# Performance work log

Measured on AMD Instinct MI355X. Metric: run time of the kernel, lower is better.

## Reference

```python
import jax, jax.numpy as jnp
import numpy as np

D_MODEL = 768
NUM_HEADS = 12
D_K = D_MODEL // NUM_HEADS
B, T = 2, 4096


def setup_inputs() -> dict:
    key = jax.random.key(0)
    ks = jax.random.split(key, 5)
    x = jax.random.normal(ks[0], (B, T, D_MODEL), dtype=jnp.float32)
    # causal mask: True = masked (matches masked_fill semantics)
    mask = jnp.triu(jnp.ones((T, T), dtype=bool), k=1)
    W_qkv = jax.random.normal(ks[1], (D_MODEL, 3 * D_MODEL), dtype=jnp.float32) / np.sqrt(D_MODEL)
    b_qkv = jax.random.normal(ks[2], (3 * D_MODEL,), dtype=jnp.float32) * 0.02
    W_out = jax.random.normal(ks[3], (D_MODEL, D_MODEL), dtype=jnp.float32) / np.sqrt(D_MODEL)
    b_out = jax.random.normal(ks[4], (D_MODEL,), dtype=jnp.float32) * 0.02
    return {"x": x, "mask": mask, "W_qkv": W_qkv, "b_qkv": b_qkv, "W_out": W_out, "b_out": b_out}


def reference(x, mask, W_qkv, b_qkv, W_out, b_out):
    Bb, Tt, C = x.shape
    qkv = x @ W_qkv + b_qkv                       # [B,T,3C]
    # torch: reshape(B,T,H,3*d_k).transpose(1,2) then chunk on last dim
    qkv = qkv.reshape(Bb, Tt, NUM_HEADS, 3, D_K)  # split each head's 3*d_k chunk
    qkv = jnp.transpose(qkv, (0, 2, 1, 3, 4))     # [B,H,T,3,d_k]
    q, k, v = qkv[..., 0, :], qkv[..., 1, :], qkv[..., 2, :]
    scores = jnp.einsum('bhqd,bhkd->bhqk', q, k) / np.sqrt(D_K)
    scores = jnp.where(mask[None, None], -jnp.inf, scores)
    attn = jax.nn.softmax(scores, axis=-1)
    context = jnp.einsum('bhqk,bhkd->bhqd', attn, v)
    context = jnp.transpose(context, (0, 2, 1, 3)).reshape(Bb, Tt, C)
    return context @ W_out + b_out
```

## Files before the change

kernel.cpp:

```cpp
#include <hip/hip_runtime.h>
#include <hip/hip_bf16.h>
#include <stdint.h>


typedef __attribute__((ext_vector_type(8))) short bf16x8;
typedef __attribute__((ext_vector_type(4))) short bf16x4;
typedef __attribute__((ext_vector_type(4))) float f32x4;

#define TT 4096
#define NH 12
#define DK 64
#define DMODEL 768
#define NQKV 2304

__device__ __forceinline__ unsigned short f2bf(float f) {
    union { float f; unsigned u; } v; v.f = f;
    unsigned u = v.u;
    return (unsigned short)((u + 0x7fffu + ((u >> 16) & 1u)) >> 16);
}
__device__ __forceinline__ unsigned fbits(float f) {
    union { float f; unsigned u; } v; v.f = f; return v.u;
}
__device__ __forceinline__ unsigned pack_bf2(float a, float b) {
    return __builtin_amdgcn_perm(fbits(b) + 0x8000u, fbits(a) + 0x8000u, 0x07060302u);
}
__device__ __forceinline__ unsigned cvt_pk_bf16(float a, float b) {
    unsigned r;
    asm("v_cvt_pk_bf16_f32 %0, %1, %2" : "=v"(r) : "v"(a), "v"(b));
    return r;
}
__device__ __forceinline__ void glds16(const void* g, void* l) {
    __builtin_amdgcn_global_load_lds(
        (const __attribute__((address_space(1))) void*)g,
        (__attribute__((address_space(3))) void*)l, 16, 0, 0);
}

__global__ __launch_bounds__(256)
void prep(const float* __restrict__ x, unsigned short* __restrict__ xb,
          const float* __restrict__ Wq, unsigned short* __restrict__ Wqt,
          const float* __restrict__ Wo, unsigned short* __restrict__ Wot) {
    int b = blockIdx.x;
    if (b < 6144) {
        int i = (b * 256 + threadIdx.x) * 4;
        float4 v = *(const float4*)(x + i);
        uint2 u;
        u.x = pack_bf2(v.x, v.y);
        u.y = pack_bf2(v.z, v.w);
        *(uint2*)(xb + i) = u;
        return;
    }
    __shared__ unsigned short tile[64][65];
    const float* W; unsigned short* Wt; int K, N, bx, by;
    if (b < 6144 + 432) {
        int bb = b - 6144; bx = bb % 36; by = bb / 36;
        W = Wq; Wt = Wqt; K = DMODEL; N = NQKV;
    } else {
        int bb = b - 6576; bx = bb % 12; by = bb / 12;
        W = Wo; Wt = Wot; K = DMODEL; N = DMODEL;
    }
    int k0 = by * 64, n0 = bx * 64;
    int c = threadIdx.x & 63;
    int r0 = threadIdx.x >> 6;
    for (int p = 0; p < 16; ++p) {
        int r = r0 + p * 4;
        tile[r][c] = f2bf(W[(size_t)(k0 + r) * N + n0 + c]);
    }
    __syncthreads();
    for (int p = 0; p < 16; ++p) {
        int n = r0 + p * 4;
        Wt[(size_t)(n0 + n) * K + k0 + c] = tile[c][n];
    }
}

__global__ __launch_bounds__(256, 3)
void gemm_qkv(const unsigned short* __restrict__ Amat, const unsigned short* __restrict__ Bmat,
              const float* __restrict__ bias, unsigned short* __restrict__ qb,
              unsigned short* __restrict__ kb, unsigned short* __restrict__ vtb) {
    __shared__ unsigned short As[192 * 64];
    __shared__ unsigned short Bs[128 * 64];
    const int K = DMODEL;
    int bid = (int)blockIdx.y * 64 + (int)blockIdx.x;
    int idx = bid >> 3;
    int n0 = ((bid & 7) * 8 + (idx & 7)) * 128;
    int m0 = (idx >> 3) * 192;
    int tid = threadIdx.x, lane = tid & 63, w = tid >> 6;
    int wm = (w >> 1) * 96, wn = (w & 1) * 64;
    int quad = lane >> 4, lc = lane & 15;

    int gc8 = ((lane & 7) ^ (lane >> 3)) * 8;
    int arow0 = w * 48 + (lane >> 3);
    int brow0 = w * 32 + (lane >> 3);
    const unsigned short* agp0 = Amat + (size_t)(m0 + arow0) * K + gc8;
    const unsigned short* bgp0 = Bmat + (size_t)(n0 + brow0) * K + gc8;
    unsigned short* alp0 = &As[w * 6 * 512];
    unsigned short* blp0 = &Bs[w * 4 * 512];

    int foff[2];
    for (int h = 0; h < 2; ++h)
        foff[h] = lc * 64 + (((quad + 4 * h) ^ (lc & 7)) * 8);

    f32x4 acc[6][4];
    for (int a = 0; a < 6; ++a)
        for (int b2 = 0; b2 < 4; ++b2) acc[a][b2] = (f32x4){0.f, 0.f, 0.f, 0.f};

    for (int k0 = 0; k0 < K; k0 += 64) {
        {
            const unsigned short* ag = agp0;
            for (int p = 0; p < 6; ++p) {
                glds16(ag, alp0 + p * 512);
                ag += 8 * DMODEL;
            }
            const unsigned short* bg = bgp0;
            for (int p = 0; p < 4; ++p) {
                glds16(bg, blp0 + p * 512);
                bg += 8 * DMODEL;
            }
            agp0 += 64; bgp0 += 64;
        }
        __syncthreads();
        bf16x8 bfr[4][2];
        for (int nt = 0; nt < 4; ++nt)
            for (int h = 0; h < 2; ++h)
                bfr[nt][h] = *(const bf16x8*)(&Bs[wn * 64 + nt * 1024 + foff[h]]);
        for (int mt = 0; mt < 6; ++mt) {
            bf16x8 af0 = *(const bf16x8*)(&As[wm * 64 + mt * 1024 + foff[0]]);
            bf16x8 af1 = *(const bf16x8*)(&As[wm * 64 + mt * 1024 + foff[1]]);
            for (int nt = 0; nt < 4; ++nt) {
                acc[mt][nt] = __builtin_amdgcn_mfma_f32_16x16x32_bf16(
                    af0, bfr[nt][0], acc[mt][nt], 0, 0, 0);
                acc[mt][nt] = __builtin_amdgcn_mfma_f32_16x16x32_bf16(
                    af1, bfr[nt][1], acc[mt][nt], 0, 0, 0);
            }
        }
        __syncthreads();
    }
    const float c2q = 0.18033688f;
    for (int mt = 0; mt < 6; ++mt) {
        int colv = m0 + wm + mt * 16 + quad * 4;
        float4 bv = *(const float4*)(bias + colv);
        int h = colv / 192;
        int r = colv - h * 192;
        int which = r >> 6;
        int d0 = r & 63;
        for (int nt = 0; nt < 4; ++nt) {
            int tok = n0 + wn + nt * 16 + lc;
            int b = tok >> 12, t = tok & 4095;
            size_t bh = (size_t)(b * NH + h);
            float v0 = acc[mt][nt][0] + bv.x, v1 = acc[mt][nt][1] + bv.y;
            float v2 = acc[mt][nt][2] + bv.z, v3 = acc[mt][nt][3] + bv.w;
            if (which == 0) {
                uint2 u;
                u.x = cvt_pk_bf16(v0 * c2q, v1 * c2q);
                u.y = cvt_pk_bf16(v2 * c2q, v3 * c2q);
                *(uint2*)(qb + (bh * TT + t) * DK + d0) = u;
            } else if (which == 1) {
                uint2 u;
                u.x = cvt_pk_bf16(v0, v1);
                u.y = cvt_pk_bf16(v2, v3);
                *(uint2*)(kb + (bh * TT + t) * DK + d0) = u;
            } else {
                unsigned short* vp = vtb + (bh * DK + d0) * TT + t;
                vp[0] = f2bf(v0); vp[TT] = f2bf(v1);
                vp[2 * TT] = f2bf(v2); vp[3 * TT] = f2bf(v3);
            }
        }
    }
}

template <bool DIAG>
__device__ __forceinline__ void flash_tile(const unsigned short* __restrict__ Kb,
                                           const unsigned short* __restrict__ Vb,
                                           bf16x8 qf0, bf16x8 qf1,
                                           f32x4 (&o)[4], f32x4& ol,
                                           int kt, int q_lo, int quad, int lc) {
    int c0 = quad ^ (lc & 7);
    int sw = lc & 7;
    const bf16x4 ones = {(short)0x3F80, (short)0x3F80, (short)0x3F80, (short)0x3F80};
    for (int ktile = 0; ktile < 4; ++ktile) {
        bf16x8 kf0 = *(const bf16x8*)(&Kb[(ktile * 16 + lc) * 64 + c0 * 8]);
        bf16x8 kf1 = *(const bf16x8*)(&Kb[(ktile * 16 + lc) * 64 + (c0 ^ 4) * 8]);
        f32x4 s = (f32x4){0.f, 0.f, 0.f, 0.f};
        __builtin_amdgcn_s_setprio(1);
        s = __builtin_amdgcn_mfma_f32_16x16x32_bf16(kf0, qf0, s, 0, 0, 0);
        s = __builtin_amdgcn_mfma_f32_16x16x32_bf16(kf1, qf1, s, 0, 0, 0);
        __builtin_amdgcn_s_setprio(0);
        float p[4];
        if (DIAG) {
            int key0 = kt + ktile * 16 + quad * 4;
            int qcol = q_lo + lc;
            for (int i = 0; i < 4; ++i) {
                float e = __builtin_amdgcn_exp2f(s[i]);
                if (key0 + i > qcol) e = 0.f;
                p[i] = e;
            }
        } else {
            for (int i = 0; i < 4; ++i) p[i] = __builtin_amdgcn_exp2f(s[i]);
        }
        union { uint2 u; bf16x4 v; } pc;
        pc.u.x = cvt_pk_bf16(p[0], p[1]);
        pc.u.y = cvt_pk_bf16(p[2], p[3]);
        int c8 = (ktile * 2 + (quad >> 1)) ^ sw;
        int voff = c8 * 8 + (quad & 1) * 4;
        __builtin_amdgcn_s_setprio(1);
        ol = __builtin_amdgcn_mfma_f32_16x16x16bf16_1k(ones, pc.v, ol, 0, 0, 0);
        for (int dt = 0; dt < 4; ++dt) {
            bf16x4 vf = *(const bf16x4*)(&Vb[(dt * 16 + lc) * 64 + voff]);
            o[dt] = __builtin_amdgcn_mfma_f32_16x16x16bf16_1k(vf, pc.v, o[dt], 0, 0, 0);
        }
        __builtin_amdgcn_s_setprio(0);
    }
}

__global__ __launch_bounds__(256)
void flash_attn(const unsigned short* __restrict__ qbuf,
                const unsigned short* __restrict__ kbuf,
                const unsigned short* __restrict__ vtbuf,
                unsigned short* __restrict__ ctx) {
    __shared__ unsigned short Ks[2][64 * 64];
    __shared__ unsigned short Vs[2][64 * 64];
    int bh = blockIdx.x;
    int qblk = 63 - (int)blockIdx.y;
    int tid = threadIdx.x, lane = tid & 63, w = tid >> 6;
    int quad = lane >> 4, lc = lane & 15;
    const size_t base = (size_t)bh * TT * DK;
    int col8 = ((lane & 7) ^ (lane >> 3)) * 8;
    size_t hb = (size_t)(bh / NH) * TT * DMODEL + (size_t)(bh % NH) * DK;

    int q_lo = qblk * 64 + w * 16;
    int ntile = qblk + 1;

    int rb = (w & 1) * 4;
    const unsigned short* sgp[4];
    int stepEls;
    if (w < 2) {
        const unsigned short* kb0 = kbuf + base + (size_t)(lane >> 3) * DK + col8;
        for (int r = 0; r < 4; ++r) sgp[r] = kb0 + (size_t)((rb + r) * 8) * DK;
        stepEls = 64 * DK;
    } else {
        const unsigned short* vb0 = vtbuf + base + (size_t)(lane >> 3) * TT + col8;
        for (int r = 0; r < 4; ++r) sgp[r] = vb0 + (size_t)((rb + r) * 8) * TT;
        stepEls = 64;
    }

    bf16x8 qf0, qf1;
    {
        const unsigned short* qp = qbuf + base + (size_t)(q_lo + lc) * DK;
        qf0 = *(const bf16x8*)(qp + quad * 8);
        qf1 = *(const bf16x8*)(qp + 32 + quad * 8);
    }
    f32x4 o[4];
    for (int dt = 0; dt < 4; ++dt) o[dt] = (f32x4){0.f, 0.f, 0.f, 0.f};
    f32x4 ol = (f32x4){0.f, 0.f, 0.f, 0.f};

    {
        if (w < 2)
            for (int r = 0; r < 4; ++r) {
                glds16(sgp[r], &Ks[0][(rb + r) * 512]);
                sgp[r] += stepEls;
            }
        else
            for (int r = 0; r < 4; ++r) {
                glds16(sgp[r], &Vs[0][(rb + r) * 512]);
                sgp[r] += stepEls;
            }
    }
    __syncthreads();

    for (int ti = 0; ti < ntile; ++ti) {
        int cur = ti & 1;
        if (ti + 1 < ntile) {
            if (w < 2)
                for (int r = 0; r < 4; ++r) {
                    glds16(sgp[r], &Ks[cur ^ 1][(rb + r) * 512]);
                    sgp[r] += stepEls;
                }
            else
                for (int r = 0; r < 4; ++r) {
                    glds16(sgp[r], &Vs[cur ^ 1][(rb + r) * 512]);
                    sgp[r] += stepEls;
                }
        }
        int kt = ti * 64;
        if (ti == ntile - 1)
            flash_tile<true>(&Ks[cur][0], &Vs[cur][0], qf0, qf1, o, ol,
                             kt, q_lo, quad, lc);
        else
            flash_tile<false>(&Ks[cur][0], &Vs[cur][0], qf0, qf1, o, ol,
                              kt, q_lo, quad, lc);
        __syncthreads();
    }

    float inv = 1.f / ol[0];
    int t = q_lo + lc;
    unsigned short* cp = ctx + hb + (size_t)t * DMODEL;
    for (int dt = 0; dt < 4; ++dt) {
        uint2 u;
        u.x = cvt_pk_bf16(o[dt][0] * inv, o[dt][1] * inv);
        u.y = cvt_pk_bf16(o[dt][2] * inv, o[dt][3] * inv);
        *(uint2*)(cp + dt * 16 + quad * 4) = u;
    }
}

__global__ __launch_bounds__(256, 4)
void gemm_out(const unsigned short* __restrict__ Amat, const unsigned short* __restrict__ Bmat,
              const float* __restrict__ bias, float* __restrict__ out) {
    __shared__ unsigned short S[(64 + 128) * 64];
    const int K = DMODEL;
    int bid = (int)blockIdx.y * 64 + (int)blockIdx.x;
    int idx = bid >> 3;
    int n0 = ((bid & 7) * 8 + (idx & 7)) * 128;
    int m0 = (idx >> 3) * 64;
    int tid = threadIdx.x, lane = tid & 63, w = tid >> 6;
    int wm = (w & 1) * 32, wn = (w >> 1) * 64;
    int quad = lane >> 4, lc = lane & 15;

    const unsigned short* gp[6]; unsigned short* lp[6];
    for (int p = 0; p < 6; ++p) {
        int c = (w * 6 + p) * 64 + lane;
        if (c < 512) {
            int row = c >> 3, gc = (c & 7) ^ (row & 7);
            gp[p] = Amat + (size_t)(m0 + row) * K + gc * 8;
        } else {
            int cb = c - 512;
            int row = cb >> 3, gc = (cb & 7) ^ (row & 7);
            gp[p] = Bmat + (size_t)(n0 + row) * K + gc * 8;
        }
        lp[p] = &S[(w * 6 + p) * 512];
    }
    int foffA[2][2], foffB[4][2];
    for (int mt = 0; mt < 2; ++mt)
        for (int h = 0; h < 2; ++h)
            foffA[mt][h] = (wm + mt * 16 + lc) * 64 + (((quad + 4 * h) ^ (lc & 7)) * 8);
    for (int nt = 0; nt < 4; ++nt)
        for (int h = 0; h < 2; ++h)
            foffB[nt][h] = 4096 + (wn + nt * 16 + lc) * 64 + (((quad + 4 * h) ^ (lc & 7)) * 8);

    f32x4 acc[2][4];
    for (int a = 0; a < 2; ++a)
        for (int b2 = 0; b2 < 4; ++b2) acc[a][b2] = (f32x4){0.f, 0.f, 0.f, 0.f};

    for (int k0 = 0; k0 < K; k0 += 64) {
        for (int p = 0; p < 6; ++p) {
            glds16(gp[p], lp[p]);
            gp[p] += 64;
        }
        __syncthreads();
        bf16x8 af[2][2], bfr[4][2];
        for (int mt = 0; mt < 2; ++mt)
            for (int h = 0; h < 2; ++h) af[mt][h] = *(const bf16x8*)(&S[foffA[mt][h]]);
        for (int nt = 0; nt < 4; ++nt)
            for (int h = 0; h < 2; ++h) bfr[nt][h] = *(const bf16x8*)(&S[foffB[nt][h]]);
        for (int mt = 0; mt < 2; ++mt)
            for (int nt = 0; nt < 4; ++nt) {
                acc[mt][nt] = __builtin_amdgcn_mfma_f32_16x16x32_bf16(
                    af[mt][0], bfr[nt][0], acc[mt][nt], 0, 0, 0);
                acc[mt][nt] = __builtin_amdgcn_mfma_f32_16x16x32_bf16(
                    af[mt][1], bfr[nt][1], acc[mt][nt], 0, 0, 0);
            }
        __syncthreads();
    }
    for (int mt = 0; mt < 2; ++mt) {
        int colv = m0 + wm + mt * 16 + quad * 4;
        float4 bv = *(const float4*)(bias + colv);
        for (int nt = 0; nt < 4; ++nt) {
            int tok = n0 + wn + nt * 16 + lc;
            float4 ov;
            ov.x = acc[mt][nt][0] + bv.x;
            ov.y = acc[mt][nt][1] + bv.y;
            ov.z = acc[mt][nt][2] + bv.z;
            ov.w = acc[mt][nt][3] + bv.w;
            *(float4*)(out + (size_t)tok * DMODEL + colv) = ov;
        }
    }
}

extern "C" void kernel_launch(void* const* d_in, const int* in_sizes, int n_in,
                              void* d_out, int out_size, void* d_ws, size_t ws_size,
                              hipStream_t stream) {
    const float* x     = (const float*)d_in[0];
    const float* W_qkv = (const float*)d_in[2];
    const float* b_qkv = (const float*)d_in[3];
    const float* W_out = (const float*)d_in[4];
    const float* b_out = (const float*)d_in[5];
    float* out = (float*)d_out;

    unsigned short* ws = (unsigned short*)d_ws;
    unsigned short* Wqkv_t = ws;
    unsigned short* Wout_t = Wqkv_t + (size_t)NQKV * DMODEL;
    unsigned short* q_buf  = Wout_t + (size_t)DMODEL * DMODEL;
    unsigned short* k_buf  = q_buf  + (size_t)2 * NH * TT * DK;
    unsigned short* vt_buf = k_buf  + (size_t)2 * NH * TT * DK;
    unsigned short* ctx    = vt_buf + (size_t)2 * NH * TT * DK;
    unsigned short* x_bf   = ctx;

    prep<<<dim3(6720), 256, 0, stream>>>(x, x_bf, W_qkv, Wqkv_t, W_out, Wout_t);
    gemm_qkv<<<dim3((2 * TT) / 128, NQKV / 192), 256, 0, stream>>>(
        Wqkv_t, x_bf, b_qkv, q_buf, k_buf, vt_buf);
    flash_attn<<<dim3(2 * NH, TT / 64), 256, 0, stream>>>(q_buf, k_buf, vt_buf, ctx);
    gemm_out<<<dim3((2 * TT) / 128, DMODEL / 64), 256, 0, stream>>>(
        Wout_t, ctx, b_out, out);
}
```

Before: 255.3 us.

## Double-buffer LDS tiles in QKV and output projection GEMMs

Both projection GEMMs now keep two LDS buffers. The next K-slice is prefetched into the spare buffer while MFMAs run on the current one, and the barrier that sat between load and compute inside the loop is removed. The aim is to hide global-to-LDS load latency behind matrix math. In exchange LDS use doubles, so the launch-bounds occupancy targets drop from 3 to 2 and from 4 to 3 blocks per CU.

```diff
diff --git a/kernel.cpp b/kernel.cpp
--- a/kernel.cpp
+++ b/kernel.cpp
@@ -72,13 +72,14 @@
     }
 }
 
-__global__ __launch_bounds__(256, 3)
+__global__ __launch_bounds__(256, 2)
 void gemm_qkv(const unsigned short* __restrict__ Amat, const unsigned short* __restrict__ Bmat,
               const float* __restrict__ bias, unsigned short* __restrict__ qb,
               unsigned short* __restrict__ kb, unsigned short* __restrict__ vtb) {
-    __shared__ unsigned short As[192 * 64];
-    __shared__ unsigned short Bs[128 * 64];
+    __shared__ unsigned short As[2][192 * 64];
+    __shared__ unsigned short Bs[2][128 * 64];
     const int K = DMODEL;
+    const int NSTEP = K / 64;
     int bid = (int)blockIdx.y * 64 + (int)blockIdx.x;
     int idx = bid >> 3;
     int n0 = ((bid & 7) * 8 + (idx & 7)) * 128;
@@ -92,8 +93,8 @@
     int brow0 = w * 32 + (lane >> 3);
     const unsigned short* agp0 = Amat + (size_t)(m0 + arow0) * K + gc8;
     const unsigned short* bgp0 = Bmat + (size_t)(n0 + brow0) * K + gc8;
-    unsigned short* alp0 = &As[w * 6 * 512];
-    unsigned short* blp0 = &Bs[w * 4 * 512];
+    int alo = w * 6 * 512;
+    int blo = w * 4 * 512;
 
     int foff[2];
     for (int h = 0; h < 2; ++h)
@@ -103,28 +104,31 @@
     for (int a = 0; a < 6; ++a)
         for (int b2 = 0; b2 < 4; ++b2) acc[a][b2] = (f32x4){0.f, 0.f, 0.f, 0.f};
 
-    for (int k0 = 0; k0 < K; k0 += 64) {
-        {
+    {
+        const unsigned short* ag = agp0;
+        for (int p = 0; p < 6; ++p) { glds16(ag, &As[0][alo + p * 512]); ag += 8 * DMODEL; }
+        const unsigned short* bg = bgp0;
+        for (int p = 0; p < 4; ++p) { glds16(bg, &Bs[0][blo + p * 512]); bg += 8 * DMODEL; }
+        agp0 += 64; bgp0 += 64;
+    }
+    __syncthreads();
+
+    for (int step = 0; step < NSTEP; ++step) {
+        int cur = step & 1;
+        if (step + 1 < NSTEP) {
             const unsigned short* ag = agp0;
-            for (int p = 0; p < 6; ++p) {
-                glds16(ag, alp0 + p * 512);
-                ag += 8 * DMODEL;
-            }
+            for (int p = 0; p < 6; ++p) { glds16(ag, &As[cur ^ 1][alo + p * 512]); ag += 8 * DMODEL; }
             const unsigned short* bg = bgp0;
-            for (int p = 0; p < 4; ++p) {
-                glds16(bg, blp0 + p * 512);
-                bg += 8 * DMODEL;
-            }
+            for (int p = 0; p < 4; ++p) { glds16(bg, &Bs[cur ^ 1][blo + p * 512]); bg += 8 * DMODEL; }
             agp0 += 64; bgp0 += 64;
         }
-        __syncthreads();
         bf16x8 bfr[4][2];
         for (int nt = 0; nt < 4; ++nt)
             for (int h = 0; h < 2; ++h)
-                bfr[nt][h] = *(const bf16x8*)(&Bs[wn * 64 + nt * 1024 + foff[h]]);
+                bfr[nt][h] = *(const bf16x8*)(&Bs[cur][wn * 64 + nt * 1024 + foff[h]]);
         for (int mt = 0; mt < 6; ++mt) {
-            bf16x8 af0 = *(const bf16x8*)(&As[wm * 64 + mt * 1024 + foff[0]]);
-            bf16x8 af1 = *(const bf16x8*)(&As[wm * 64 + mt * 1024 + foff[1]]);
+            bf16x8 af0 = *(const bf16x8*)(&As[cur][wm * 64 + mt * 1024 + foff[0]]);
+            bf16x8 af1 = *(const bf16x8*)(&As[cur][wm * 64 + mt * 1024 + foff[1]]);
             for (int nt = 0; nt < 4; ++nt) {
                 acc[mt][nt] = __builtin_amdgcn_mfma_f32_16x16x32_bf16(
                     af0, bfr[nt][0], acc[mt][nt], 0, 0, 0);
@@ -301,11 +305,12 @@
     }
 }
 
-__global__ __launch_bounds__(256, 4)
+__global__ __launch_bounds__(256, 3)
 void gemm_out(const unsigned short* __restrict__ Amat, const unsigned short* __restrict__ Bmat,
               const float* __restrict__ bias, float* __restrict__ out) {
-    __shared__ unsigned short S[(64 + 128) * 64];
+    __shared__ unsigned short S[2][(64 + 128) * 64];
     const int K = DMODEL;
+    const int NSTEP = K / 64;
     int bid = (int)blockIdx.y * 64 + (int)blockIdx.x;
     int idx = bid >> 3;
     int n0 = ((bid & 7) * 8 + (idx & 7)) * 128;
@@ -314,7 +319,7 @@
     int wm = (w & 1) * 32, wn = (w >> 1) * 64;
     int quad = lane >> 4, lc = lane & 15;
 
-    const unsigned short* gp[6]; unsigned short* lp[6];
+    const unsigned short* gp[6]; int lpo[6];
     for (int p = 0; p < 6; ++p) {
         int c = (w * 6 + p) * 64 + lane;
         if (c < 512) {
@@ -325,7 +330,7 @@
             int row = cb >> 3, gc = (cb & 7) ^ (row & 7);
             gp[p] = Bmat + (size_t)(n0 + row) * K + gc * 8;
         }
-        lp[p] = &S[(w * 6 + p) * 512];
+        lpo[p] = (w * 6 + p) * 512;
     }
     int foffA[2][2], foffB[4][2];
     for (int mt = 0; mt < 2; ++mt)
@@ -339,17 +344,27 @@
     for (int a = 0; a < 2; ++a)
         for (int b2 = 0; b2 < 4; ++b2) acc[a][b2] = (f32x4){0.f, 0.f, 0.f, 0.f};
 
-    for (int k0 = 0; k0 < K; k0 += 64) {
+    {
         for (int p = 0; p < 6; ++p) {
-            glds16(gp[p], lp[p]);
+            glds16(gp[p], &S[0][lpo[p]]);
             gp[p] += 64;
         }
-        __syncthreads();
+    }
+    __syncthreads();
+
+    for (int step = 0; step < NSTEP; ++step) {
+        int cur = step & 1;
+        if (step + 1 < NSTEP) {
+            for (int p = 0; p < 6; ++p) {
+                glds16(gp[p], &S[cur ^ 1][lpo[p]]);
+                gp[p] += 64;
+            }
+        }
         bf16x8 af[2][2], bfr[4][2];
         for (int mt = 0; mt < 2; ++mt)
-            for (int h = 0; h < 2; ++h) af[mt][h] = *(const bf16x8*)(&S[foffA[mt][h]]);
+            for (int h = 0; h < 2; ++h) af[mt][h] = *(const bf16x8*)(&S[cur][foffA[mt][h]]);
         for (int nt = 0; nt < 4; ++nt)
-            for (int h = 0; h < 2; ++h) bfr[nt][h] = *(const bf16x8*)(&S[foffB[nt][h]]);
+            for (int h = 0; h < 2; ++h) bfr[nt][h] = *(const bf16x8*)(&S[cur][foffB[nt][h]]);
         for (int mt = 0; mt < 2; ++mt)
             for (int nt = 0; nt < 4; ++nt) {
                 acc[mt][nt] = __builtin_amdgcn_mfma_f32_16x16x32_bf16(
```

Measured after the change: 271.7 us. 6.4% more time.
